# Performance work log

Measured on AMD Instinct MI355X. Metric: run time of the kernel, lower is better.

## Reference

```python
import jax, jax.numpy as jnp
import numpy as np

LAMBDA_SCR = 0.015
LAMBDA_IFD = 0.015


def setup_inputs() -> dict:
    key = jax.random.key(0)
    k = jax.random.split(key, 5)
    pred = jax.random.normal(k[0], (32, 1000), dtype=jnp.float32)
    feat0 = jax.random.normal(k[1], (32, 64, 128, 128), dtype=jnp.float32)
    feat1 = jax.random.normal(k[2], (32, 128, 64, 64), dtype=jnp.float32)
    feat2 = jax.random.normal(k[3], (32, 256, 32, 32), dtype=jnp.float32)  # teacher
    target = jax.random.randint(k[4], (32,), 0, 1000, dtype=jnp.int64)
    return {"pred": pred, "feat0": feat0, "feat1": feat1, "feat2": feat2, "target": target}


def _adaptive_avg_pool2d(x, out_hw):
    # Exact-multiple adaptive average pool (matches torch for integer ratios).
    B, C, H, W = x.shape
    Ho, Wo = out_hw
    if Ho >= H:
        x = jnp.repeat(x, Ho // H, axis=2)  # replication upsample
    else:
        x = x.reshape(B, C, Ho, H // Ho, W).mean(axis=3)
    if Wo >= W:
        x = jnp.repeat(x, Wo // W, axis=3)
    else:
        x = x.reshape(B, C, x.shape[2], Wo, W // Wo).mean(axis=4)
    return x


def _random_channel_selection(feat, target_channels, key):
    C = feat.shape[1]
    if C == target_channels:
        return feat
    idx = jax.random.permutation(key, C)[:target_channels]
    return feat[:, idx, :, :]


def _ifd_loss(feat):
    B, C, H, W = feat.shape
    if C < 2:
        return jnp.float32(0.0)
    # L2 norm per channel -> descending sort of channel indices
    norms = jnp.linalg.norm(feat.reshape(B, C, H * W), axis=-1)  # [B, C]
    idx = jnp.argsort(-norms, axis=1)                            # [B, C]
    half = C // 2
    strong = jnp.take_along_axis(feat, idx[:, :half, None, None], axis=1)
    weak = jnp.take_along_axis(feat, idx[:, half:2 * half, None, None], axis=1)
    A_strong = jax.nn.sigmoid(strong.mean(axis=1))  # [B, H, W]
    A_weak = jax.nn.sigmoid(weak.mean(axis=1))
    # sum_b mean_hw(diff^2) / B == mean over all elements
    return jnp.mean((A_weak - jax.lax.stop_gradient(A_strong)) ** 2)


def reference(pred, feat0, feat1, feat2, target):
    logp = jax.nn.log_softmax(pred, axis=-1)
    l_main = -jnp.mean(jnp.take_along_axis(logp, target[:, None], axis=1))

    features = [feat0, feat1, feat2]
    teacher = features[-1]
    students = features[:-1]

    sel_key = jax.random.key(42)  # fixed keys stand in for torch.randperm
    l_scr = jnp.float32(0.0)
    for i, student in enumerate(students):
        t_down = _adaptive_avg_pool2d(teacher, student.shape[2:])
        min_C = min(teacher.shape[1], student.shape[1])
        ks, kt = jax.random.split(jax.random.fold_in(sel_key, i))
        s_aligned = _random_channel_selection(student, min_C, ks)
        t_aligned = _random_channel_selection(t_down, min_C, kt)
        l_scr = l_scr + jnp.mean((s_aligned - jax.lax.stop_gradient(t_aligned)) ** 2)
    l_scr = l_scr / len(students)

    l_ifd = jnp.float32(0.0)
    for feat in features:
        l_ifd = l_ifd + _ifd_loss(feat)
    l_ifd = l_ifd / len(features)

    total = l_main + LAMBDA_SCR * l_scr + LAMBDA_IFD * l_ifd
    return (total, l_main, l_scr, l_ifd)
```

## Files before the change

### kernel.cpp

```cpp
#include <hip/hip_runtime.h>
#include <stdint.h>
#include <math.h>

#define NB 32

__device__ __forceinline__ void tf_block(uint32_t k0, uint32_t k1, uint32_t& x0, uint32_t& x1) {
  uint32_t k2 = 0x1BD11BDAu ^ k0 ^ k1;
  x0 += k0; x1 += k1;
#define TFR(r) { x0 += x1; x1 = (x1 << r) | (x1 >> (32 - r)); x1 ^= x0; }
  TFR(13) TFR(15) TFR(26) TFR(6)
  x0 += k1; x1 += k2 + 1u;
  TFR(17) TFR(29) TFR(16) TFR(24)
  x0 += k2; x1 += k0 + 2u;
  TFR(13) TFR(15) TFR(26) TFR(6)
  x0 += k0; x1 += k1 + 3u;
  TFR(17) TFR(29) TFR(16) TFR(24)
  x0 += k1; x1 += k2 + 4u;
  TFR(13) TFR(15) TFR(26) TFR(6)
  x0 += k2; x1 += k0 + 5u;
#undef TFR
}

__device__ __forceinline__ float sigmoidf(float x) { return 1.0f / (1.0f + expf(-x)); }

__device__ __forceinline__ float wave_reduce(float v) {
  for (int o = 32; o > 0; o >>= 1) v += __shfl_down(v, o, 64);
  return v;
}

__global__ __launch_bounds__(256) void k0_perm(int* idx0, int* idx1, float* ws) {
  __shared__ uint32_t sub[2][2];
  __shared__ uint32_t bits[2][256];
  int t = threadIdx.x;
  for (int i = t; i < 384; i += 256) ws[i] = 0.0f;
  if (t == 0) {
    for (int i = 0; i < 2; ++i) {
      uint32_t f0 = 0u, f1 = (uint32_t)i;
      tf_block(0u, 42u, f0, f1);
      uint32_t a0 = 0u, a1 = 2u; tf_block(f0, f1, a0, a1);
      uint32_t b0 = 1u, b1 = 3u; tf_block(f0, f1, b0, b1);
      uint32_t kt0 = a1, kt1 = b1;
      uint32_t c0 = 0u, c1 = 2u; tf_block(kt0, kt1, c0, c1);
      uint32_t d0 = 1u, d1 = 3u; tf_block(kt0, kt1, d0, d1);
      sub[i][0] = c1; sub[i][1] = d1;
    }
  }
  __syncthreads();
  if (t < 128) {
    for (int i = 0; i < 2; ++i) {
      uint32_t x0 = (uint32_t)t, x1 = (uint32_t)(t + 128);
      tf_block(sub[i][0], sub[i][1], x0, x1);
      bits[i][t] = x0; bits[i][t + 128] = x1;
    }
  }
  __syncthreads();
  for (int i = 0; i < 2; ++i) {
    uint32_t mine = bits[i][t];
    int rank = 0;
    for (int k = 0; k < 256; ++k) {
      uint32_t v = bits[i][k];
      rank += (v < mine) || (v == mine && k < t);
    }
    int lim = (i == 0) ? 64 : 128;
    if (rank < lim) { (i == 0 ? idx0 : idx1)[rank] = t; }
  }
}

__global__ __launch_bounds__(256) void k1_pass1(
    const float* __restrict__ f0, const float* __restrict__ f1, const float* __restrict__ f2,
    const int* __restrict__ idx0, const int* __restrict__ idx1,
    float* __restrict__ ns0, float* __restrict__ ns1, float* __restrict__ ns2,
    float* __restrict__ scr0_s, float* __restrict__ scr1_s) {
  __shared__ float tpl[4096];
  __shared__ float red[8];
  int bid = blockIdx.x;
  int lane = threadIdx.x & 63, wv = threadIdx.x >> 6;
  if (bid < 2048) {
    int b = bid >> 6, c = bid & 63;
    int tc = idx0[c];
    ((float4*)tpl)[threadIdx.x] = ((const float4*)(f2 + ((size_t)b * 256 + tc) * 1024))[threadIdx.x];
    __syncthreads();
    const float4* plane = (const float4*)(f0 + (size_t)bid * 16384);
    float ssq = 0.f, scr = 0.f;
#pragma unroll 8
    for (int it = 0; it < 16; ++it) {
      int p = (wv * 16 + it) * 64 + lane;
      float4 v = plane[p];
      int pix = p * 4, h = pix >> 7, w = pix & 127;
      float tv = tpl[(h >> 2) * 32 + (w >> 2)];
      ssq += v.x * v.x + v.y * v.y + v.z * v.z + v.w * v.w;
      float dx = v.x - tv, dy = v.y - tv, dz = v.z - tv, dw = v.w - tv;
      scr += dx * dx + dy * dy + dz * dz + dw * dw;
    }
    ssq = wave_reduce(ssq); scr = wave_reduce(scr);
    if (lane == 0) { red[wv] = ssq; red[4 + wv] = scr; }
    __syncthreads();
    if (threadIdx.x == 0) {
      ns0[bid] = red[0] + red[1] + red[2] + red[3];
      atomicAdd(&scr0_s[bid & 63], red[4] + red[5] + red[6] + red[7]);
    }
  } else if (bid < 3072) {
    int unit = ((bid - 2048) << 2) + wv;
    int b = unit >> 7, c = unit & 127;
    int tc = idx1[c];
    const float4* tp = (const float4*)(f2 + ((size_t)b * 256 + tc) * 1024);
#pragma unroll
    for (int it = 0; it < 4; ++it)
      ((float4*)tpl)[(wv << 8) + it * 64 + lane] = tp[it * 64 + lane];
    __syncthreads();
    const float* mytpl = tpl + (wv << 10);
    const float4* plane = (const float4*)(f1 + (size_t)unit * 4096);
    float ssq = 0.f, scr = 0.f;
#pragma unroll 8
    for (int it = 0; it < 16; ++it) {
      int p = it * 64 + lane;
      float4 v = plane[p];
      int pix = p * 4, h = pix >> 6, w = pix & 63;
      int tb = (h >> 1) * 32 + (w >> 1);
      float t0 = mytpl[tb], t1 = mytpl[tb + 1];
      ssq += v.x * v.x + v.y * v.y + v.z * v.z + v.w * v.w;
      float dx = v.x - t0, dy = v.y - t0, dz = v.z - t1, dw = v.w - t1;
      scr += dx * dx + dy * dy + dz * dz + dw * dw;
    }
    ssq = wave_reduce(ssq); scr = wave_reduce(scr);
    if (lane == 0) {
      ns1[unit] = ssq;
      atomicAdd(&scr1_s[unit & 63], scr);
    }
  } else {
    int u4 = ((bid - 3072) << 2) + wv;
    int p0 = u4 << 2;
#pragma unroll
    for (int j = 0; j < 4; ++j) {
      const float4* plane = (const float4*)(f2 + (size_t)(p0 + j) * 1024);
      float ssq = 0.f;
#pragma unroll
      for (int it = 0; it < 4; ++it) {
        float4 v = plane[it * 64 + lane];
        ssq += v.x * v.x + v.y * v.y + v.z * v.z + v.w * v.w;
      }
      ssq = wave_reduce(ssq);
      if (lane == 0) ns2[p0 + j] = ssq;
    }
  }
}

template<int C>
__device__ __forceinline__ void rank_work(const float* __restrict__ normsq,
                                          float* __restrict__ flags, int b, float* nm) {
  for (int c = threadIdx.x; c < C; c += 256) nm[c] = sqrtf(normsq[b * C + c]);
  __syncthreads();
  for (int c = threadIdx.x; c < C; c += 256) {
    float mine = nm[c];
    int rank = 0;
    for (int k = 0; k < C; ++k) {
      float v = nm[k];
      rank += (v > mine) || (v == mine && k < c);
    }
    flags[b * C + c] = (rank < C / 2) ? 1.0f : 0.0f;
  }
}

__device__ __forceinline__ void main_work(const float* __restrict__ pred,
                                          const int* __restrict__ target,
                                          float* acc, int b, float* sh) {
  int t = threadIdx.x;
  const float* row = pred + b * 1000;
  float m = -INFINITY;
  for (int j = t; j < 1000; j += 256) m = fmaxf(m, row[j]);
  sh[t] = m; __syncthreads();
  for (int s = 128; s > 0; s >>= 1) { if (t < s) sh[t] = fmaxf(sh[t], sh[t + s]); __syncthreads(); }
  m = sh[0]; __syncthreads();
  float e = 0.f;
  for (int j = t; j < 1000; j += 256) e += expf(row[j] - m);
  sh[t] = e; __syncthreads();
  for (int s = 128; s > 0; s >>= 1) { if (t < s) sh[t] += sh[t + s]; __syncthreads(); }
  if (t == 0) atomicAdd(acc, (logf(sh[0]) + m - row[target[b]]) * (1.0f / 32.0f));
}

__global__ __launch_bounds__(256) void k2_rank_main(
    const float* __restrict__ ns0, const float* __restrict__ ns1, const float* __restrict__ ns2,
    float* __restrict__ fl0, float* __restrict__ fl1, float* __restrict__ fl2,
    const float* __restrict__ pred, const int* __restrict__ target, float* main_acc) {
  __shared__ float sh[256];
  int bid = blockIdx.x;
  if (bid < 32)       rank_work<64 >(ns0, fl0, bid,      sh);
  else if (bid < 64)  rank_work<128>(ns1, fl1, bid - 32, sh);
  else if (bid < 96)  rank_work<256>(ns2, fl2, bid - 64, sh);
  else                main_work(pred, target, main_acc, bid - 96, sh);
}

__global__ __launch_bounds__(256) void k3_pass2(
    const float* __restrict__ f0, const float* __restrict__ f1, const float* __restrict__ f2,
    const float* __restrict__ fl0, const float* __restrict__ fl1, const float* __restrict__ fl2,
    float* __restrict__ ifd0_s, float* __restrict__ ifd1_s, float* __restrict__ ifd2_s) {
  __shared__ float fls[1024];
  int bid = blockIdx.x;
  int lane = threadIdx.x & 63, wv = threadIdx.x >> 6;
  if (bid < 512) {
    int unit = (bid << 2) + wv;
    int b = unit >> 6, chunk = unit & 63;
    float* fl = fls + (wv << 8);
    fl[lane] = fl0[(b << 6) + lane];
    const float* base = f0 + (size_t)b * 64 * 16384 + (size_t)chunk * 256;
    float4 tot = {0, 0, 0, 0}, str = {0, 0, 0, 0};
#pragma unroll 8
    for (int c = 0; c < 64; ++c) {
      float4 v = ((const float4*)(base + (size_t)c * 16384))[lane];
      float f = fl[c];
      tot.x += v.x; tot.y += v.y; tot.z += v.z; tot.w += v.w;
      str.x = fmaf(v.x, f, str.x); str.y = fmaf(v.y, f, str.y);
      str.z = fmaf(v.z, f, str.z); str.w = fmaf(v.w, f, str.w);
    }
    const float ih = 1.0f / 32.0f;
    float s = 0.f, d;
    d = sigmoidf((tot.x - str.x) * ih) - sigmoidf(str.x * ih); s += d * d;
    d = sigmoidf((tot.y - str.y) * ih) - sigmoidf(str.y * ih); s += d * d;
    d = sigmoidf((tot.z - str.z) * ih) - sigmoidf(str.z * ih); s += d * d;
    d = sigmoidf((tot.w - str.w) * ih) - sigmoidf(str.w * ih); s += d * d;
    s = wave_reduce(s);
    if (lane == 0) atomicAdd(&ifd0_s[unit & 63], s);
  } else if (bid < 640) {
    int unit = ((bid - 512) << 2) + wv;
    int b = unit >> 4, chunk = unit & 15;
    float* fl = fls + (wv << 8);
    fl[lane] = fl1[(b << 7) + lane];
    fl[64 + lane] = fl1[(b << 7) + 64 + lane];
    const float* base = f1 + (size_t)b * 128 * 4096 + (size_t)chunk * 256;
    float4 tot = {0, 0, 0, 0}, str = {0, 0, 0, 0};
#pragma unroll 8
    for (int c = 0; c < 128; ++c) {
      float4 v = ((const float4*)(base + (size_t)c * 4096))[lane];
      float f = fl[c];
      tot.x += v.x; tot.y += v.y; tot.z += v.z; tot.w += v.w;
      str.x = fmaf(v.x, f, str.x); str.y = fmaf(v.y, f, str.y);
      str.z = fmaf(v.z, f, str.z); str.w = fmaf(v.w, f, str.w);
    }
    const float ih = 1.0f / 64.0f;
    float s = 0.f, d;
    d = sigmoidf((tot.x - str.x) * ih) - sigmoidf(str.x * ih); s += d * d;
    d = sigmoidf((tot.y - str.y) * ih) - sigmoidf(str.y * ih); s += d * d;
    d = sigmoidf((tot.z - str.z) * ih) - sigmoidf(str.z * ih); s += d * d;
    d = sigmoidf((tot.w - str.w) * ih) - sigmoidf(str.w * ih); s += d * d;
    s = wave_reduce(s);
    if (lane == 0) atomicAdd(&ifd1_s[unit & 63], s);
  } else {
    int unit = ((bid - 640) << 2) + wv;
    int b = unit >> 4, chunk = unit & 15;
    float* fl = fls + (wv << 8);
#pragma unroll
    for (int k = 0; k < 4; ++k) fl[k * 64 + lane] = fl2[(b << 8) + k * 64 + lane];
    const float* base = f2 + (size_t)b * 256 * 1024 + (size_t)chunk * 64 + lane;
    float tot = 0.f, str = 0.f;
#pragma unroll 8
    for (int c = 0; c < 256; ++c) {
      float v = base[(size_t)c << 10];
      tot += v; str = fmaf(v, fl[c], str);
    }
    const float ih = 1.0f / 128.0f;
    float d = sigmoidf((tot - str) * ih) - sigmoidf(str * ih);
    float s = wave_reduce(d * d);
    if (lane == 0) atomicAdd(&ifd2_s[unit & 63], s);
  }
}

__global__ void k4_finalize(const float* __restrict__ ws, float* __restrict__ out) {
  float scr0 = 0.f, scr1 = 0.f, ifd0 = 0.f, ifd1 = 0.f, ifd2 = 0.f;
  for (int i = 0; i < 64; ++i) {
    scr0 += ws[i];       scr1 += ws[64 + i];
    ifd0 += ws[128 + i]; ifd1 += ws[192 + i]; ifd2 += ws[256 + i];
  }
  float l_main = ws[320];
  scr0 *= (1.0f / (32.0f * 64.0f * 128.0f * 128.0f));
  scr1 *= (1.0f / (32.0f * 128.0f * 64.0f * 64.0f));
  float l_scr = 0.5f * (scr0 + scr1);
  ifd0 *= (1.0f / (32.0f * 128.0f * 128.0f));
  ifd1 *= (1.0f / (32.0f * 64.0f * 64.0f));
  ifd2 *= (1.0f / (32.0f * 32.0f * 32.0f));
  float l_ifd = (ifd0 + ifd1 + ifd2) * (1.0f / 3.0f);
  float total = l_main + 0.015f * l_scr + 0.015f * l_ifd;
  out[0] = total; out[1] = l_main; out[2] = l_scr; out[3] = l_ifd;
}

extern "C" void kernel_launch(void* const* d_in, const int* in_sizes, int n_in,
                              void* d_out, int out_size, void* d_ws, size_t ws_size,
                              hipStream_t stream) {
  (void)in_sizes; (void)n_in; (void)out_size; (void)ws_size;
  const float* pred   = (const float*)d_in[0];
  const float* feat0  = (const float*)d_in[1];
  const float* feat1  = (const float*)d_in[2];
  const float* feat2  = (const float*)d_in[3];
  const int*   target = (const int*)d_in[4];
  float* out = (float*)d_out;

  float* ws = (float*)d_ws;
  float* scr0_s = ws;
  float* scr1_s = ws + 64;
  float* ifd0_s = ws + 128;
  float* ifd1_s = ws + 192;
  float* ifd2_s = ws + 256;
  float* main_a = ws + 320;
  int*   idx0 = (int*)(ws + 384);
  int*   idx1 = idx0 + 64;
  float* ns0  = (float*)(idx1 + 128);
  float* ns1  = ns0 + 2048;
  float* ns2  = ns1 + 4096;
  float* fl0  = ns2 + 8192;
  float* fl1  = fl0 + 2048;
  float* fl2  = fl1 + 4096;

  k0_perm<<<1, 256, 0, stream>>>(idx0, idx1, ws);
  k1_pass1<<<3584, 256, 0, stream>>>(feat0, feat1, feat2, idx0, idx1, ns0, ns1, ns2, scr0_s, scr1_s);
  k2_rank_main<<<128, 256, 0, stream>>>(ns0, ns1, ns2, fl0, fl1, fl2, pred, target, main_a);
  k3_pass2<<<768, 256, 0, stream>>>(feat0, feat1, feat2, fl0, fl1, fl2, ifd0_s, ifd1_s, ifd2_s);
  k4_finalize<<<1, 1, 0, stream>>>(ws, out);
}
```

Baseline: 339.1 us.

## Precompute channel sums in pass 1 and read only strong channels in pass 2

Pass 1 is reorganised to walk spatial chunks across all channels. It accumulates per-pixel channel totals into a workspace buffer and builds per-channel squared norms with wave reductions and atomics. Rank now emits a list of the strong channel indices instead of 0/1 flags, so pass 2 gathers and sums only the strong half of the channels and reads the precomputed totals. This is meant to halve the feature traffic in the second pass. In exchange it adds writing and reading the totals buffer, many per-channel atomics and a larger workspace clear, and pass 1 runs far fewer blocks.

```diff
diff --git a/kernel.cpp b/kernel.cpp
--- a/kernel.cpp
+++ b/kernel.cpp
@@ -1,8 +1,6 @@
 #include <hip/hip_runtime.h>
 #include <stdint.h>
 #include <math.h>
-
-#define NB 32
 
 __device__ __forceinline__ void tf_block(uint32_t k0, uint32_t k1, uint32_t& x0, uint32_t& x1) {
   uint32_t k2 = 0x1BD11BDAu ^ k0 ^ k1;
@@ -32,7 +30,7 @@
   __shared__ uint32_t sub[2][2];
   __shared__ uint32_t bits[2][256];
   int t = threadIdx.x;
-  for (int i = t; i < 384; i += 256) ws[i] = 0.0f;
+  for (int i = t; i < 14912; i += 256) ws[i] = 0.0f;
   if (t == 0) {
     for (int i = 0; i < 2; ++i) {
       uint32_t f0 = 0u, f1 = (uint32_t)i;
@@ -70,84 +68,102 @@
     const float* __restrict__ f0, const float* __restrict__ f1, const float* __restrict__ f2,
     const int* __restrict__ idx0, const int* __restrict__ idx1,
     float* __restrict__ ns0, float* __restrict__ ns1, float* __restrict__ ns2,
+    float* __restrict__ tot0, float* __restrict__ tot1, float* __restrict__ tot2,
     float* __restrict__ scr0_s, float* __restrict__ scr1_s) {
   __shared__ float tpl[4096];
+  __shared__ int sidx[128];
   __shared__ float red[8];
-  int bid = blockIdx.x;
-  int lane = threadIdx.x & 63, wv = threadIdx.x >> 6;
-  if (bid < 2048) {
-    int b = bid >> 6, c = bid & 63;
-    int tc = idx0[c];
-    ((float4*)tpl)[threadIdx.x] = ((const float4*)(f2 + ((size_t)b * 256 + tc) * 1024))[threadIdx.x];
-    __syncthreads();
-    const float4* plane = (const float4*)(f0 + (size_t)bid * 16384);
-    float ssq = 0.f, scr = 0.f;
-#pragma unroll 8
-    for (int it = 0; it < 16; ++it) {
-      int p = (wv * 16 + it) * 64 + lane;
-      float4 v = plane[p];
-      int pix = p * 4, h = pix >> 7, w = pix & 127;
-      float tv = tpl[(h >> 2) * 32 + (w >> 2)];
-      ssq += v.x * v.x + v.y * v.y + v.z * v.z + v.w * v.w;
-      float dx = v.x - tv, dy = v.y - tv, dz = v.z - tv, dw = v.w - tv;
+  int bid = blockIdx.x, tid = threadIdx.x;
+  int lane = tid & 63, wv = tid >> 6;
+  if (bid < 256) {
+    int b = bid >> 3, chunk = bid & 7;
+    if (tid < 128) sidx[tid] = idx1[tid];
+    float2 tot = {0.f, 0.f};
+    float scr = 0.f;
+    int tbase = (tid >> 6) * 32 + (tid & 31);
+    for (int g = 0; g < 4; ++g) {
+      __syncthreads();
+      {
+        int cl = tid >> 3, part = tid & 7;
+        int tc = sidx[g * 32 + cl];
+        const float4* src = (const float4*)(f2 + ((size_t)(b * 256 + tc)) * 1024 + chunk * 128);
+        float4* dst = (float4*)(tpl + cl * 128);
+#pragma unroll
+        for (int j = 0; j < 4; ++j) dst[part * 4 + j] = src[part * 4 + j];
+      }
+      __syncthreads();
+#pragma unroll 8
+      for (int j = 0; j < 32; ++j) {
+        int c = g * 32 + j;
+        float2 v = ((const float2*)(f1 + ((size_t)(b * 128 + c)) * 4096 + chunk * 512))[tid];
+        float t = tpl[j * 128 + tbase];
+        tot.x += v.x; tot.y += v.y;
+        float dx = v.x - t, dy = v.y - t;
+        scr += dx * dx + dy * dy;
+        float ssq = wave_reduce(v.x * v.x + v.y * v.y);
+        if (lane == 0) atomicAdd(&ns1[b * 128 + c], ssq);
+      }
+    }
+    ((float2*)(tot1 + (size_t)b * 4096 + chunk * 512))[tid] = tot;
+    scr = wave_reduce(scr);
+    if (lane == 0) red[wv] = scr;
+    __syncthreads();
+    if (tid == 0) atomicAdd(&scr1_s[bid & 63], red[0] + red[1] + red[2] + red[3]);
+  } else if (bid < 384) {
+    int unit = bid - 256;
+    int b = unit >> 2, chunk = unit & 3;
+    float4 tot = {0.f, 0.f, 0.f, 0.f};
+    int c0 = wv << 6;
+#pragma unroll 8
+    for (int j = 0; j < 64; ++j) {
+      int c = c0 + j;
+      float4 v = ((const float4*)(f2 + ((size_t)(b * 256 + c)) * 1024 + chunk * 256))[lane];
+      tot.x += v.x; tot.y += v.y; tot.z += v.z; tot.w += v.w;
+      float ssq = wave_reduce(v.x * v.x + v.y * v.y + v.z * v.z + v.w * v.w);
+      if (lane == 0) atomicAdd(&ns2[b * 256 + c], ssq);
+    }
+    ((float4*)(tpl + (wv << 10)))[lane] = tot;
+    __syncthreads();
+    float val = tpl[tid] + tpl[1024 + tid] + tpl[2048 + tid] + tpl[3072 + tid];
+    tot2[(size_t)b * 1024 + chunk * 256 + tid] = val;
+  } else {
+    int unit = bid - 384;
+    int b = unit >> 4, chunk = unit & 15;
+    if (tid < 64) sidx[tid] = idx0[tid];
+    __syncthreads();
+    {
+      int c = tid >> 2, q = tid & 3;
+      int tc = sidx[c];
+      const float4* src = (const float4*)(f2 + ((size_t)(b * 256 + tc)) * 1024 + chunk * 64);
+      float4* dst = (float4*)(tpl + c * 64);
+#pragma unroll
+      for (int j = 0; j < 4; ++j) dst[q * 4 + j] = src[q * 4 + j];
+    }
+    __syncthreads();
+    float4 tot = {0.f, 0.f, 0.f, 0.f};
+    float scr = 0.f;
+    int tbase = (tid >> 7) * 32 + (tid & 31);
+#pragma unroll 8
+    for (int c = 0; c < 64; ++c) {
+      float4 v = ((const float4*)(f0 + ((size_t)(b * 64 + c)) * 16384 + chunk * 1024))[tid];
+      float t = tpl[c * 64 + tbase];
+      tot.x += v.x; tot.y += v.y; tot.z += v.z; tot.w += v.w;
+      float dx = v.x - t, dy = v.y - t, dz = v.z - t, dw = v.w - t;
       scr += dx * dx + dy * dy + dz * dz + dw * dw;
-    }
-    ssq = wave_reduce(ssq); scr = wave_reduce(scr);
-    if (lane == 0) { red[wv] = ssq; red[4 + wv] = scr; }
-    __syncthreads();
-    if (threadIdx.x == 0) {
-      ns0[bid] = red[0] + red[1] + red[2] + red[3];
-      atomicAdd(&scr0_s[bid & 63], red[4] + red[5] + red[6] + red[7]);
-    }
-  } else if (bid < 3072) {
-    int unit = ((bid - 2048) << 2) + wv;
-    int b = unit >> 7, c = unit & 127;
-    int tc = idx1[c];
-    const float4* tp = (const float4*)(f2 + ((size_t)b * 256 + tc) * 1024);
-#pragma unroll
-    for (int it = 0; it < 4; ++it)
-      ((float4*)tpl)[(wv << 8) + it * 64 + lane] = tp[it * 64 + lane];
-    __syncthreads();
-    const float* mytpl = tpl + (wv << 10);
-    const float4* plane = (const float4*)(f1 + (size_t)unit * 4096);
-    float ssq = 0.f, scr = 0.f;
-#pragma unroll 8
-    for (int it = 0; it < 16; ++it) {
-      int p = it * 64 + lane;
-      float4 v = plane[p];
-      int pix = p * 4, h = pix >> 6, w = pix & 63;
-      int tb = (h >> 1) * 32 + (w >> 1);
-      float t0 = mytpl[tb], t1 = mytpl[tb + 1];
-      ssq += v.x * v.x + v.y * v.y + v.z * v.z + v.w * v.w;
-      float dx = v.x - t0, dy = v.y - t0, dz = v.z - t1, dw = v.w - t1;
-      scr += dx * dx + dy * dy + dz * dz + dw * dw;
-    }
-    ssq = wave_reduce(ssq); scr = wave_reduce(scr);
-    if (lane == 0) {
-      ns1[unit] = ssq;
-      atomicAdd(&scr1_s[unit & 63], scr);
-    }
-  } else {
-    int u4 = ((bid - 3072) << 2) + wv;
-    int p0 = u4 << 2;
-#pragma unroll
-    for (int j = 0; j < 4; ++j) {
-      const float4* plane = (const float4*)(f2 + (size_t)(p0 + j) * 1024);
-      float ssq = 0.f;
-#pragma unroll
-      for (int it = 0; it < 4; ++it) {
-        float4 v = plane[it * 64 + lane];
-        ssq += v.x * v.x + v.y * v.y + v.z * v.z + v.w * v.w;
-      }
-      ssq = wave_reduce(ssq);
-      if (lane == 0) ns2[p0 + j] = ssq;
-    }
+      float ssq = wave_reduce(v.x * v.x + v.y * v.y + v.z * v.z + v.w * v.w);
+      if (lane == 0) atomicAdd(&ns0[b * 64 + c], ssq);
+    }
+    ((float4*)(tot0 + (size_t)b * 16384 + chunk * 1024))[tid] = tot;
+    scr = wave_reduce(scr);
+    if (lane == 0) red[wv] = scr;
+    __syncthreads();
+    if (tid == 0) atomicAdd(&scr0_s[bid & 63], red[0] + red[1] + red[2] + red[3]);
   }
 }
 
 template<int C>
 __device__ __forceinline__ void rank_work(const float* __restrict__ normsq,
-                                          float* __restrict__ flags, int b, float* nm) {
+                                          int* __restrict__ sl, int b, float* nm) {
   for (int c = threadIdx.x; c < C; c += 256) nm[c] = sqrtf(normsq[b * C + c]);
   __syncthreads();
   for (int c = threadIdx.x; c < C; c += 256) {
@@ -157,7 +173,7 @@
       float v = nm[k];
       rank += (v > mine) || (v == mine && k < c);
     }
-    flags[b * C + c] = (rank < C / 2) ? 1.0f : 0.0f;
+    if (rank < C / 2) sl[b * (C / 2) + rank] = c;
   }
 }
 
@@ -180,38 +196,37 @@
 
 __global__ __launch_bounds__(256) void k2_rank_main(
     const float* __restrict__ ns0, const float* __restrict__ ns1, const float* __restrict__ ns2,
-    float* __restrict__ fl0, float* __restrict__ fl1, float* __restrict__ fl2,
+    int* __restrict__ sl0, int* __restrict__ sl1, int* __restrict__ sl2,
     const float* __restrict__ pred, const int* __restrict__ target, float* main_acc) {
   __shared__ float sh[256];
   int bid = blockIdx.x;
-  if (bid < 32)       rank_work<64 >(ns0, fl0, bid,      sh);
-  else if (bid < 64)  rank_work<128>(ns1, fl1, bid - 32, sh);
-  else if (bid < 96)  rank_work<256>(ns2, fl2, bid - 64, sh);
+  if (bid < 32)       rank_work<64 >(ns0, sl0, bid,      sh);
+  else if (bid < 64)  rank_work<128>(ns1, sl1, bid - 32, sh);
+  else if (bid < 96)  rank_work<256>(ns2, sl2, bid - 64, sh);
   else                main_work(pred, target, main_acc, bid - 96, sh);
 }
 
 __global__ __launch_bounds__(256) void k3_pass2(
     const float* __restrict__ f0, const float* __restrict__ f1, const float* __restrict__ f2,
-    const float* __restrict__ fl0, const float* __restrict__ fl1, const float* __restrict__ fl2,
+    const int* __restrict__ sl0, const int* __restrict__ sl1, const int* __restrict__ sl2,
+    const float* __restrict__ tot0, const float* __restrict__ tot1, const float* __restrict__ tot2,
     float* __restrict__ ifd0_s, float* __restrict__ ifd1_s, float* __restrict__ ifd2_s) {
-  __shared__ float fls[1024];
+  __shared__ int sls[512];
   int bid = blockIdx.x;
   int lane = threadIdx.x & 63, wv = threadIdx.x >> 6;
+  int* ml = sls + (wv << 7);
   if (bid < 512) {
     int unit = (bid << 2) + wv;
     int b = unit >> 6, chunk = unit & 63;
-    float* fl = fls + (wv << 8);
-    fl[lane] = fl0[(b << 6) + lane];
-    const float* base = f0 + (size_t)b * 64 * 16384 + (size_t)chunk * 256;
-    float4 tot = {0, 0, 0, 0}, str = {0, 0, 0, 0};
-#pragma unroll 8
-    for (int c = 0; c < 64; ++c) {
-      float4 v = ((const float4*)(base + (size_t)c * 16384))[lane];
-      float f = fl[c];
-      tot.x += v.x; tot.y += v.y; tot.z += v.z; tot.w += v.w;
-      str.x = fmaf(v.x, f, str.x); str.y = fmaf(v.y, f, str.y);
-      str.z = fmaf(v.z, f, str.z); str.w = fmaf(v.w, f, str.w);
-    }
+    if (lane < 32) ml[lane] = sl0[b * 32 + lane];
+    float4 str = {0.f, 0.f, 0.f, 0.f};
+#pragma unroll 8
+    for (int j = 0; j < 32; ++j) {
+      int c = ml[j];
+      float4 v = ((const float4*)(f0 + ((size_t)(b * 64 + c)) * 16384 + chunk * 256))[lane];
+      str.x += v.x; str.y += v.y; str.z += v.z; str.w += v.w;
+    }
+    float4 tot = ((const float4*)(tot0 + (size_t)b * 16384 + chunk * 256))[lane];
     const float ih = 1.0f / 32.0f;
     float s = 0.f, d;
     d = sigmoidf((tot.x - str.x) * ih) - sigmoidf(str.x * ih); s += d * d;
@@ -223,19 +238,15 @@
   } else if (bid < 640) {
     int unit = ((bid - 512) << 2) + wv;
     int b = unit >> 4, chunk = unit & 15;
-    float* fl = fls + (wv << 8);
-    fl[lane] = fl1[(b << 7) + lane];
-    fl[64 + lane] = fl1[(b << 7) + 64 + lane];
-    const float* base = f1 + (size_t)b * 128 * 4096 + (size_t)chunk * 256;
-    float4 tot = {0, 0, 0, 0}, str = {0, 0, 0, 0};
-#pragma unroll 8
-    for (int c = 0; c < 128; ++c) {
-      float4 v = ((const float4*)(base + (size_t)c * 4096))[lane];
-      float f = fl[c];
-      tot.x += v.x; tot.y += v.y; tot.z += v.z; tot.w += v.w;
-      str.x = fmaf(v.x, f, str.x); str.y = fmaf(v.y, f, str.y);
-      str.z = fmaf(v.z, f, str.z); str.w = fmaf(v.w, f, str.w);
-    }
+    ml[lane] = sl1[b * 64 + lane];
+    float4 str = {0.f, 0.f, 0.f, 0.f};
+#pragma unroll 8
+    for (int j = 0; j < 64; ++j) {
+      int c = ml[j];
+      float4 v = ((const float4*)(f1 + ((size_t)(b * 128 + c)) * 4096 + chunk * 256))[lane];
+      str.x += v.x; str.y += v.y; str.z += v.z; str.w += v.w;
+    }
+    float4 tot = ((const float4*)(tot1 + (size_t)b * 4096 + chunk * 256))[lane];
     const float ih = 1.0f / 64.0f;
     float s = 0.f, d;
     d = sigmoidf((tot.x - str.x) * ih) - sigmoidf(str.x * ih); s += d * d;
@@ -246,20 +257,24 @@
     if (lane == 0) atomicAdd(&ifd1_s[unit & 63], s);
   } else {
     int unit = ((bid - 640) << 2) + wv;
-    int b = unit >> 4, chunk = unit & 15;
-    float* fl = fls + (wv << 8);
-#pragma unroll
-    for (int k = 0; k < 4; ++k) fl[k * 64 + lane] = fl2[(b << 8) + k * 64 + lane];
-    const float* base = f2 + (size_t)b * 256 * 1024 + (size_t)chunk * 64 + lane;
-    float tot = 0.f, str = 0.f;
-#pragma unroll 8
-    for (int c = 0; c < 256; ++c) {
-      float v = base[(size_t)c << 10];
-      tot += v; str = fmaf(v, fl[c], str);
-    }
+    int b = unit >> 2, chunk = unit & 3;
+    ml[lane] = sl2[b * 128 + lane];
+    ml[64 + lane] = sl2[b * 128 + 64 + lane];
+    float4 str = {0.f, 0.f, 0.f, 0.f};
+#pragma unroll 8
+    for (int j = 0; j < 128; ++j) {
+      int c = ml[j];
+      float4 v = ((const float4*)(f2 + ((size_t)(b * 256 + c)) * 1024 + chunk * 256))[lane];
+      str.x += v.x; str.y += v.y; str.z += v.z; str.w += v.w;
+    }
+    float4 tot = ((const float4*)(tot2 + (size_t)b * 1024 + chunk * 256))[lane];
     const float ih = 1.0f / 128.0f;
-    float d = sigmoidf((tot - str) * ih) - sigmoidf(str * ih);
-    float s = wave_reduce(d * d);
+    float s = 0.f, d;
+    d = sigmoidf((tot.x - str.x) * ih) - sigmoidf(str.x * ih); s += d * d;
+    d = sigmoidf((tot.y - str.y) * ih) - sigmoidf(str.y * ih); s += d * d;
+    d = sigmoidf((tot.z - str.z) * ih) - sigmoidf(str.z * ih); s += d * d;
+    d = sigmoidf((tot.w - str.w) * ih) - sigmoidf(str.w * ih); s += d * d;
+    s = wave_reduce(s);
     if (lane == 0) atomicAdd(&ifd2_s[unit & 63], s);
   }
 }
@@ -301,17 +316,22 @@
   float* ifd2_s = ws + 256;
   float* main_a = ws + 320;
   int*   idx0 = (int*)(ws + 384);
-  int*   idx1 = idx0 + 64;
-  float* ns0  = (float*)(idx1 + 128);
-  float* ns1  = ns0 + 2048;
-  float* ns2  = ns1 + 4096;
-  float* fl0  = ns2 + 8192;
-  float* fl1  = fl0 + 2048;
-  float* fl2  = fl1 + 4096;
+  int*   idx1 = (int*)(ws + 448);
+  float* ns0  = ws + 576;
+  float* ns1  = ws + 2624;
+  float* ns2  = ws + 6720;
+  int*   sl0  = (int*)(ws + 14912);
+  int*   sl1  = (int*)(ws + 15936);
+  int*   sl2  = (int*)(ws + 17984);
+  float* tot0 = ws + 22080;
+  float* tot1 = ws + 546368;
+  float* tot2 = ws + 677440;
 
   k0_perm<<<1, 256, 0, stream>>>(idx0, idx1, ws);
-  k1_pass1<<<3584, 256, 0, stream>>>(feat0, feat1, feat2, idx0, idx1, ns0, ns1, ns2, scr0_s, scr1_s);
-  k2_rank_main<<<128, 256, 0, stream>>>(ns0, ns1, ns2, fl0, fl1, fl2, pred, target, main_a);
-  k3_pass2<<<768, 256, 0, stream>>>(feat0, feat1, feat2, fl0, fl1, fl2, ifd0_s, ifd1_s, ifd2_s);
+  k1_pass1<<<896, 256, 0, stream>>>(feat0, feat1, feat2, idx0, idx1,
+                                    ns0, ns1, ns2, tot0, tot1, tot2, scr0_s, scr1_s);
+  k2_rank_main<<<128, 256, 0, stream>>>(ns0, ns1, ns2, sl0, sl1, sl2, pred, target, main_a);
+  k3_pass2<<<672, 256, 0, stream>>>(feat0, feat1, feat2, sl0, sl1, sl2,
+                                    tot0, tot1, tot2, ifd0_s, ifd1_s, ifd2_s);
   k4_finalize<<<1, 1, 0, stream>>>(ws, out);
 }
```

After: 369.8 us. 1.09x slower.
